# Performance work log

Measured on AMD Instinct MI355X. Metric: run time of the kernel, lower is better.

## Reference

```python
import jax, jax.numpy as jnp
import numpy as np

HIDDEN = 2048
NUM_HEADS = 16
HEAD_DIM = HIDDEN // NUM_HEADS


def setup_inputs() -> dict:
    key = jax.random.key(0)
    k1, k2, k3 = jax.random.split(key, 3)
    B, S = 2, 2048
    hidden_states = jax.random.normal(k1, (B, S, HIDDEN), dtype=jnp.float32)
    attention_mask = jnp.zeros((B, 1, 1, S), dtype=jnp.float32)
    W_qkv = jax.random.normal(k2, (HIDDEN, 3 * HIDDEN), dtype=jnp.float32) * (1.0 / np.sqrt(HIDDEN))
    b_qkv = jnp.zeros((3 * HIDDEN,), dtype=jnp.float32)
    W_out = jax.random.normal(k3, (HIDDEN, HIDDEN), dtype=jnp.float32) * (1.0 / np.sqrt(HIDDEN))
    b_out = jnp.zeros((HIDDEN,), dtype=jnp.float32)
    return {"hidden_states": hidden_states, "attention_mask": attention_mask,
            "W_qkv": W_qkv, "b_qkv": b_qkv, "W_out": W_out, "b_out": b_out}


def reference(hidden_states, attention_mask, W_qkv, b_qkv, W_out, b_out):
    B, S, H = hidden_states.shape
    scale = 1.0 / np.sqrt(HEAD_DIM)
    # fused QKV projection (column-parallel linear, world_size=1)
    mixed = hidden_states @ W_qkv + b_qkv                      # [B,S,3H]
    q, k, v = jnp.split(mixed, 3, axis=-1)
    # [B, heads, S, head_dim]
    q = q.reshape(B, S, NUM_HEADS, HEAD_DIM).transpose(0, 2, 1, 3)
    k = k.reshape(B, S, NUM_HEADS, HEAD_DIM).transpose(0, 2, 1, 3)
    v = v.reshape(B, S, NUM_HEADS, HEAD_DIM).transpose(0, 2, 1, 3)
    scores = jnp.einsum('bhqd,bhkd->bhqk', q, k) * scale       # [B,h,S,S]
    scores = scores + attention_mask                            # additive mask broadcast
    probs = jax.nn.softmax(scores, axis=-1)
    ctx = jnp.einsum('bhqk,bhkd->bhqd', probs, v)               # [B,h,S,d]
    ctx = ctx.transpose(0, 2, 1, 3).reshape(B, S, H)
    return ctx @ W_out + b_out
```

## Files before the change

### kernel.cpp

```cpp
#include <hip/hip_runtime.h>
#include <hip/hip_bf16.h>
#include <stdint.h>

typedef __attribute__((ext_vector_type(4)))  float   f32x4;
typedef __attribute__((ext_vector_type(16))) float   f32x16;
typedef __attribute__((ext_vector_type(8)))  __bf16  bf16x8;
typedef __attribute__((ext_vector_type(8)))  short   s16x8;
typedef __attribute__((ext_vector_type(4)))  unsigned short u16x4;
typedef __attribute__((ext_vector_type(4)))  float   fl4;
typedef __attribute__((ext_vector_type(2)))  unsigned int u32x2;
typedef __attribute__((ext_vector_type(4)))  unsigned int u32x4;

#define DEVFN static __device__ __forceinline__

constexpr int BATCH = 2, SEQ = 2048, HID = 2048, NHEAD = 16, HDIM = 128;
constexpr int MROWS = BATCH * SEQ;
constexpr int N3    = 3 * HID;
constexpr float LOG2E = 1.44269504088896340736f;
constexpr float SCALE_LOG2E = 0.12751649736170852f;
constexpr float DEFER_THR = 11.541560327111708f;

DEVFN unsigned short f2bf(float f) {
  unsigned int u = __float_as_uint(f);
  u += 0x7FFFu + ((u >> 16) & 1u);
  return (unsigned short)(u >> 16);
}

DEVFN void async_cp16(const void* g, void* l) {
  __builtin_amdgcn_global_load_lds(
      (__attribute__((address_space(1))) void*)g,
      (__attribute__((address_space(3))) void*)l, 16, 0, 0);
}

DEVFN f32x4 mfma_bf16(bf16x8 a, bf16x8 b, f32x4 c) {
  return __builtin_amdgcn_mfma_f32_16x16x32_bf16(a, b, c, 0, 0, 0);
}
DEVFN f32x16 mfma32(bf16x8 a, bf16x8 b, f32x16 c) {
  return __builtin_amdgcn_mfma_f32_32x32x16_bf16(a, b, c, 0, 0, 0);
}
DEVFN unsigned cvt_pk_bf16(float lo, float hi) {
  unsigned r;
  asm("v_cvt_pk_bf16_f32 %0, %1, %2" : "=v"(r) : "v"(lo), "v"(hi));
  return r;
}

__global__ __launch_bounds__(256) void cvt_bf16(const float* __restrict__ x,
                                                unsigned short* __restrict__ hi, int n4) {
  for (int i = blockIdx.x * blockDim.x + threadIdx.x; i < n4; i += gridDim.x * blockDim.x) {
    fl4 v = ((const fl4*)x)[i];
    u16x4 h;
#pragma unroll
    for (int j = 0; j < 4; j++) h[j] = f2bf(v[j]);
    ((u16x4*)hi)[i] = h;
  }
}

__global__ __launch_bounds__(256) void cvt_transpose(const float* __restrict__ W,
                                                     unsigned short* __restrict__ T,
                                                     int R, int C) {
  __shared__ float tile[32][33];
  const int c0 = blockIdx.x * 32, r0 = blockIdx.y * 32;
  const int tx = threadIdx.x, ty = threadIdx.y;
#pragma unroll
  for (int i = 0; i < 4; i++) tile[ty + 8 * i][tx] = W[(size_t)(r0 + ty + 8 * i) * C + c0 + tx];
  __syncthreads();
#pragma unroll
  for (int i = 0; i < 4; i++) {
    const float v = tile[tx][ty + 8 * i];
    T[(size_t)(c0 + ty + 8 * i) * R + r0 + tx] = f2bf(v);
  }
}

template <bool OUT_BF16>
__global__ __launch_bounds__(512, 1) void gemm_ring(const unsigned short* __restrict__ A,
                                                    const unsigned short* __restrict__ Bt,
                                                    const float* __restrict__ bias,
                                                    void* __restrict__ Cout, int Ndim) {
  constexpr int KDIM  = 2048;
  constexpr int NT    = KDIM / 64;
  constexpr int ASLOT = 256 * 64;
  constexpr int BSLOT = 128 * 64;
  constexpr int SLOT  = ASLOT + BSLOT;
  __shared__ __align__(16) unsigned short smem[3 * SLOT];

  const int tid = threadIdx.x;
  const int wid = tid >> 6, lane = tid & 63;
  const int wm = wid >> 2, wn = wid & 3;
  const int g = lane >> 4, q = lane & 15;
  const int n0 = blockIdx.x * 128, m0 = blockIdx.y * 256;

  const int srow = (wid << 3) + (lane >> 3);
  const int scol = (((lane & 7) ^ (lane >> 3)) << 4);
  const char* gA = (const char*)A  + ((size_t)(m0 + srow) * KDIM) * 2 + scol;
  const char* gB = (const char*)Bt + ((size_t)(n0 + srow) * KDIM) * 2 + scol;
  const int dbase = ((wid << 3)) << 7;

  f32x4 acc[8][2] = {};
  const int axor = (q & 7) << 4;

  auto STAGE = [&](int tt, int slot) {
    char* sA = (char*)(smem + slot * SLOT);
    char* sB = (char*)(smem + slot * SLOT + ASLOT);
    const size_t koff = (size_t)tt << 7;
#pragma unroll
    for (int i = 0; i < 4; i++)
      async_cp16(gA + (size_t)(i * 64) * (KDIM * 2) + koff, sA + dbase + (i << 13));
#pragma unroll
    for (int i = 0; i < 2; i++)
      async_cp16(gB + (size_t)(i * 64) * (KDIM * 2) + koff, sB + dbase + (i << 13));
  };

  auto COMPUTE = [&](int slot) {
    const char* sA = (const char*)(smem + slot * SLOT);
    const char* sB = (const char*)(smem + slot * SLOT + ASLOT);
#pragma unroll
    for (int ks = 0; ks < 2; ks++) {
      const int kb = (ks << 6) + (g << 4);
      bf16x8 av[8], bv[2];
#pragma unroll
      for (int nf = 0; nf < 2; nf++) {
        const int row = (wn << 5) + (nf << 4) + q;
        bv[nf] = *(const bf16x8*)(sB + (row << 7) + (kb ^ axor));
      }
#pragma unroll
      for (int mf = 0; mf < 8; mf++) {
        const int row = (wm << 7) + (mf << 4) + q;
        av[mf] = *(const bf16x8*)(sA + (row << 7) + (kb ^ axor));
      }
#pragma unroll
      for (int mf = 0; mf < 8; mf++)
#pragma unroll
        for (int nf = 0; nf < 2; nf++)
          acc[mf][nf] = mfma_bf16(av[mf], bv[nf], acc[mf][nf]);
    }
  };

  STAGE(0, 0);
  STAGE(1, 1);
  int s2 = 2, sc = 0;
#pragma unroll 1
  for (int t = 0; t < NT - 2; ++t) {
    asm volatile("s_waitcnt vmcnt(6)" ::: "memory");
    __builtin_amdgcn_s_barrier();
    asm volatile("" ::: "memory");
    STAGE(t + 2, s2);
    COMPUTE(sc);
    s2 = (s2 == 2) ? 0 : s2 + 1;
    sc = (sc == 2) ? 0 : sc + 1;
  }
  asm volatile("s_waitcnt vmcnt(6)" ::: "memory");
  __builtin_amdgcn_s_barrier();
  asm volatile("" ::: "memory");
  COMPUTE(sc);
  sc = (sc == 2) ? 0 : sc + 1;
  asm volatile("s_waitcnt vmcnt(0)" ::: "memory");
  __builtin_amdgcn_s_barrier();
  asm volatile("" ::: "memory");
  COMPUTE(sc);

  float bvv[2];
#pragma unroll
  for (int nf = 0; nf < 2; nf++) bvv[nf] = bias[n0 + (wn << 5) + (nf << 4) + q];
#pragma unroll
  for (int mf = 0; mf < 8; mf++) {
    const int rowg = m0 + (wm << 7) + (mf << 4) + (g << 2);
#pragma unroll
    for (int nf = 0; nf < 2; nf++) {
      const int colg = n0 + (wn << 5) + (nf << 4) + q;
#pragma unroll
      for (int r = 0; r < 4; r++) {
        const float v = acc[mf][nf][r] + bvv[nf];
        if (OUT_BF16)
          ((unsigned short*)Cout)[(size_t)(rowg + r) * Ndim + colg] = f2bf(v);
        else
          ((float*)Cout)[(size_t)(rowg + r) * Ndim + colg] = v;
      }
    }
  }
}

__global__ __launch_bounds__(256) void transpose_v(const unsigned short* __restrict__ qkv,
                                                   unsigned short* __restrict__ vt) {
  __shared__ __align__(16) unsigned short tile[64][136];
  const int z = blockIdx.y, b = z >> 4, h = z & 15;
  const int s0 = blockIdx.x << 6;
  const int t = threadIdx.x;
#pragma unroll
  for (int i = 0; i < 4; i++) {
    const int idx = t + (i << 8);
    const int row = idx >> 4, ch = idx & 15;
    *(s16x8*)&tile[row][ch << 3] =
        *(const s16x8*)(qkv + (size_t)(b * SEQ + s0 + row) * N3 + 2 * HID + h * HDIM + (ch << 3));
  }
  __syncthreads();
#pragma unroll
  for (int i = 0; i < 4; i++) {
    const int idx = t + (i << 8);
    const int d = idx >> 3, sc = idx & 7;
    s16x8 v;
#pragma unroll
    for (int j = 0; j < 8; j++) v[j] = (short)tile[(sc << 3) + j][d];
    *(s16x8*)(vt + (size_t)(z * HDIM + d) * SEQ + s0 + (sc << 3)) = v;
  }
}

__global__ __launch_bounds__(256, 2) void attn_kernel(const unsigned short* __restrict__ qkv,
                                                      const unsigned short* __restrict__ vt,
                                                      const float* __restrict__ mask,
                                                      unsigned short* __restrict__ ctx) {
  constexpr int NT    = SEQ / 64;
  constexpr int KSLOT = 64 * 128;
  constexpr int VSLOT = 64 * 128;
  constexpr int SLOT  = KSLOT + VSLOT;
  __shared__ __align__(16) unsigned short sKV[2 * SLOT];
  __shared__ __align__(16) float sM[SEQ];

  const int bid = blockIdx.x;
  const int idx = bid >> 3;
  const int z  = ((bid & 7) << 2) + (idx >> 4);
  const int qb = idx & 15;
  const int b = z >> 4, h = z & 15;
  const int tid = threadIdx.x, wid = tid >> 6, lane = tid & 63;
  const int l31 = lane & 31, hi = lane >> 5;
  const int q0w = (qb << 7) + (wid << 5);

#pragma unroll
  for (int j = 0; j < 2; j++) {
    fl4 m = ((const fl4*)(mask + (size_t)b * SEQ))[tid + (j << 8)];
    m *= LOG2E;
    ((fl4*)sM)[tid + (j << 8)] = m;
  }

  bf16x8 bq[8];
  {
    const char* qrow = (const char*)(qkv + (size_t)(b * SEQ + q0w + l31) * N3 + h * HDIM);
#pragma unroll
    for (int kc = 0; kc < 8; kc++) bq[kc] = *(const bf16x8*)(qrow + (kc << 5) + (hi << 4));
  }

  f32x16 acc2[4] = {};
  float mrun = -1e30f, lrun = 0.f;

  const char* gK = (const char*)qkv + ((size_t)(b * SEQ) * N3 + HID + h * HDIM) * 2;
  const char* gV = (const char*)vt + ((size_t)z * HDIM * SEQ) * 2;

  auto STAGE = [&](int tt, int slot) {
    char* kb_ = (char*)(sKV + slot * SLOT);
    char* vb_ = kb_ + KSLOT * 2;
    const int k0 = tt << 6;
#pragma unroll
    for (int i = 0; i < 4; i++) {
      const int row = (i << 4) + (wid << 2) + (lane >> 4);
      const int sl  = lane & 15;
      const int dst = (i << 12) + (wid << 10);
      async_cp16(gK + ((size_t)(k0 + row) * N3) * 2 + (((sl ^ (row & 15))) << 4),
                 kb_ + dst);
      const int sv  = sl ^ (row & 15);
      const int dhi = sv >> 3, kc8 = sv & 7;
      async_cp16(gV + ((size_t)((dhi << 6) + row) * SEQ + k0 + (kc8 << 3)) * 2,
                 vb_ + dst);
    }
  };

  auto COMPUTE = [&](int t, int slot) {
    const char* sK = (const char*)(sKV + slot * SLOT);
    const char* sV = (const char*)(sKV + slot * SLOT + KSLOT);
    const int k0 = t << 6;

    f32x16 accs[2] = {};
    __builtin_amdgcn_s_setprio(1);
#pragma unroll
    for (int kb = 0; kb < 2; kb++)
#pragma unroll
      for (int kc = 0; kc < 8; kc++) {
        const int key = (kb << 5) + l31;
        const bf16x8 ka = *(const bf16x8*)(sK + (key << 8) +
                                           ((((kc << 1) + hi) ^ (l31 & 15)) << 4));
        accs[kb] = mfma32(ka, bq[kc], accs[kb]);
      }
    __builtin_amdgcn_s_setprio(0);

    float p_[2][16];
#pragma unroll
    for (int kb = 0; kb < 2; kb++) {
      fl4 mk[4];
#pragma unroll
      for (int m = 0; m < 4; m++) mk[m] = *(const fl4*)&sM[k0 + (kb << 5) + (m << 3) + (hi << 2)];
#pragma unroll
      for (int r = 0; r < 16; r++)
        p_[kb][r] = fmaf(accs[kb][r], SCALE_LOG2E, mk[r >> 2][r & 3]);
    }
    float mt = p_[0][0];
#pragma unroll
    for (int kb = 0; kb < 2; kb++)
#pragma unroll
      for (int r = 0; r < 16; r++) mt = fmaxf(mt, p_[kb][r]);
    mt = fmaxf(mt, __shfl_xor(mt, 32));
    if (!__all(mt <= mrun + DEFER_THR)) {
      const float mnew = fmaxf(mrun, mt);
      const float fs = exp2f(mrun - mnew);
      lrun *= fs;
#pragma unroll
      for (int r = 0; r < 16; r++) {
        const int qr = (r & 3) + ((r >> 2) << 3) + (hi << 2);
        const float fr = __shfl(fs, (lane & 32) | qr);
#pragma unroll
        for (int db = 0; db < 4; db++) acc2[db][r] *= fr;
      }
      mrun = mnew;
    }
    float ps = 0.f;
#pragma unroll
    for (int kb = 0; kb < 2; kb++)
#pragma unroll
      for (int r = 0; r < 16; r++) {
        const float e = exp2f(p_[kb][r] - mrun);
        p_[kb][r] = e;
        ps += e;
      }
    ps += __shfl_xor(ps, 32);
    lrun += ps;

    bf16x8 pa[4];
#pragma unroll
    for (int kb = 0; kb < 2; kb++)
#pragma unroll
      for (int hh = 0; hh < 2; hh++) {
        const float* pp = &p_[kb][hh << 3];
        const unsigned x01 = cvt_pk_bf16(pp[0], pp[1]);
        const unsigned x23 = cvt_pk_bf16(pp[2], pp[3]);
        const unsigned y01 = cvt_pk_bf16(pp[4], pp[5]);
        const unsigned y23 = cvt_pk_bf16(pp[6], pp[7]);
        const u32x2 sa = __builtin_amdgcn_permlane32_swap(x01, y01, false, false);
        const u32x2 sb = __builtin_amdgcn_permlane32_swap(x23, y23, false, false);
        const u32x4 w = {sa[0], sb[0], sa[1], sb[1]};
        pa[(kb << 1) + hh] = __builtin_bit_cast(bf16x8, w);
      }

    __builtin_amdgcn_s_setprio(1);
#pragma unroll
    for (int db = 0; db < 4; db++) {
      const int dd = ((db & 1) << 5) + l31;
#pragma unroll
      for (int ks = 0; ks < 4; ks++) {
        const int sv = ((db >> 1) << 3) + (ks << 1) + hi;
        const bf16x8 bv = *(const bf16x8*)(sV + (dd << 8) + ((sv ^ (l31 & 15)) << 4));
        acc2[db] = mfma32(pa[ks], bv, acc2[db]);
      }
    }
    __builtin_amdgcn_s_setprio(0);
  };

  STAGE(0, 0);
  __syncthreads();
#pragma unroll 1
  for (int t = 0; t < NT - 1; ++t) {
    STAGE(t + 1, (t + 1) & 1);
    COMPUTE(t, t & 1);
    asm volatile("s_waitcnt vmcnt(0)" ::: "memory");
    __builtin_amdgcn_s_barrier();
    asm volatile("" ::: "memory");
  }
  COMPUTE(NT - 1, (NT - 1) & 1);

  const float inv = 1.f / lrun;
#pragma unroll
  for (int r = 0; r < 16; r++) {
    const int qr = (r & 3) + ((r >> 2) << 3) + (hi << 2);
    const float fr = __shfl(inv, (lane & 32) | qr);
    unsigned short* crow = ctx + (size_t)(b * SEQ + q0w + qr) * HID + h * HDIM + l31;
#pragma unroll
    for (int db = 0; db < 4; db++) crow[db << 5] = f2bf(acc2[db][r] * fr);
  }
}

extern "C" void kernel_launch(void* const* d_in, const int* in_sizes, int n_in,
                              void* d_out, int out_size, void* d_ws, size_t ws_size,
                              hipStream_t stream) {
  const float* hs   = (const float*)d_in[0];
  const float* mask = (const float*)d_in[1];
  const float* Wqkv = (const float*)d_in[2];
  const float* bqkv = (const float*)d_in[3];
  const float* Wout = (const float*)d_in[4];
  const float* bout = (const float*)d_in[5];

  char* ws = (char*)d_ws;
  size_t off = 0;
  auto alloc = [&](size_t n) { char* p = ws + off; off += (n + 255) & ~(size_t)255; return p; };
  unsigned short* hs_bf = (unsigned short*)alloc((size_t)MROWS * HID * 2);
  unsigned short* wq_bf = (unsigned short*)alloc((size_t)N3 * HID * 2);
  unsigned short* wo_bf = (unsigned short*)alloc((size_t)HID * HID * 2);
  unsigned short* qkvb  = (unsigned short*)alloc((size_t)MROWS * N3 * 2);
  unsigned short* vtb   = (unsigned short*)alloc((size_t)BATCH * NHEAD * HDIM * SEQ * 2);
  unsigned short* ctxb  = (unsigned short*)alloc((size_t)MROWS * HID * 2);
  (void)ws_size;

  cvt_bf16<<<2048, 256, 0, stream>>>(hs, hs_bf, MROWS * HID / 4);
  dim3 tb(32, 8);
  cvt_transpose<<<dim3(N3 / 32, HID / 32), tb, 0, stream>>>(Wqkv, wq_bf, HID, N3);
  cvt_transpose<<<dim3(HID / 32, HID / 32), tb, 0, stream>>>(Wout, wo_bf, HID, HID);
  gemm_ring<true ><<<dim3(N3 / 128, MROWS / 256), 512, 0, stream>>>(hs_bf, wq_bf, bqkv, qkvb, N3);
  transpose_v<<<dim3(SEQ / 64, BATCH * NHEAD), 256, 0, stream>>>(qkvb, vtb);
  attn_kernel<<<512, 256, 0, stream>>>(qkvb, vtb, mask, ctxb);
  gemm_ring<false><<<dim3(HID / 128, MROWS / 256), 512, 0, stream>>>(ctxb, wo_bf, bout, (float*)d_out, HID);
}
```

Before: 267.1 us.

## Interleave GEMM tile staging with MFMA phases using ping-pong barriers and priorities

Splits the GEMM compute into four phases, each loading its A fragments from LDS, issuing part of the next tile's async global-to-LDS copies, then running MFMAs at raised wave priority between barriers. The aim is to spread memory issue across the compute so loads overlap MFMA work instead of being issued in one burst before it. The cost is several extra barriers and full lgkmcnt waits per k-step, which may serialize waves and reduce latency hiding.

New measurement: 270.4 us. Within noise of the previous version (+1.2%).

```diff
diff --git a/kernel.cpp b/kernel.cpp
--- a/kernel.cpp
+++ b/kernel.cpp
@@ -110,28 +110,53 @@
       async_cp16(gB + (size_t)(i * 64) * (KDIM * 2) + koff, sB + dbase + (i << 13));
   };
 
-  auto COMPUTE = [&](int slot) {
+  auto COMPUTE = [&](int slot, int tstage, int sstage, bool doStage) {
     const char* sA = (const char*)(smem + slot * SLOT);
     const char* sB = (const char*)(smem + slot * SLOT + ASLOT);
-#pragma unroll
-    for (int ks = 0; ks < 2; ks++) {
-      const int kb = (ks << 6) + (g << 4);
-      bf16x8 av[8], bv[2];
-#pragma unroll
-      for (int nf = 0; nf < 2; nf++) {
-        const int row = (wn << 5) + (nf << 4) + q;
-        bv[nf] = *(const bf16x8*)(sB + (row << 7) + (kb ^ axor));
-      }
-#pragma unroll
-      for (int mf = 0; mf < 8; mf++) {
-        const int row = (wm << 7) + (mf << 4) + q;
-        av[mf] = *(const bf16x8*)(sA + (row << 7) + (kb ^ axor));
-      }
-#pragma unroll
-      for (int mf = 0; mf < 8; mf++)
+    char* snA = (char*)(smem + sstage * SLOT);
+    char* snB = (char*)(smem + sstage * SLOT + ASLOT);
+    const size_t koff = (size_t)tstage << 7;
+    bf16x8 bv[2][2];
+#pragma unroll
+    for (int p = 0; p < 4; p++) {
+      if (p == 0) {
 #pragma unroll
         for (int nf = 0; nf < 2; nf++)
-          acc[mf][nf] = mfma_bf16(av[mf], bv[nf], acc[mf][nf]);
+#pragma unroll
+          for (int kk = 0; kk < 2; kk++) {
+            const int row = (wn << 5) + (nf << 4) + q;
+            bv[nf][kk] = *(const bf16x8*)(sB + (row << 7) + (((kk << 6) + (g << 4)) ^ axor));
+          }
+      }
+      bf16x8 av[2][2];
+#pragma unroll
+      for (int i = 0; i < 2; i++)
+#pragma unroll
+        for (int kk = 0; kk < 2; kk++) {
+          const int row = (wm << 7) + (((p << 1) + i) << 4) + q;
+          av[i][kk] = *(const bf16x8*)(sA + (row << 7) + (((kk << 6) + (g << 4)) ^ axor));
+        }
+      if (doStage) {
+        if (p < 2) {
+          async_cp16(gA + (size_t)((p * 2) * 64) * (KDIM * 2) + koff, snA + dbase + ((p * 2) << 13));
+          async_cp16(gA + (size_t)((p * 2 + 1) * 64) * (KDIM * 2) + koff, snA + dbase + ((p * 2 + 1) << 13));
+        } else {
+          async_cp16(gB + (size_t)((p - 2) * 64) * (KDIM * 2) + koff, snB + dbase + ((p - 2) << 13));
+        }
+      }
+      __builtin_amdgcn_s_barrier();
+      asm volatile("s_waitcnt lgkmcnt(0)" ::: "memory");
+      __builtin_amdgcn_sched_barrier(0);
+      __builtin_amdgcn_s_setprio(1);
+#pragma unroll
+      for (int i = 0; i < 2; i++)
+#pragma unroll
+        for (int nf = 0; nf < 2; nf++)
+#pragma unroll
+          for (int kk = 0; kk < 2; kk++)
+            acc[(p << 1) + i][nf] = mfma_bf16(av[i][kk], bv[nf][kk], acc[(p << 1) + i][nf]);
+      __builtin_amdgcn_s_setprio(0);
+      __builtin_amdgcn_s_barrier();
     }
   };
 
@@ -143,20 +168,19 @@
     asm volatile("s_waitcnt vmcnt(6)" ::: "memory");
     __builtin_amdgcn_s_barrier();
     asm volatile("" ::: "memory");
-    STAGE(t + 2, s2);
-    COMPUTE(sc);
+    COMPUTE(sc, t + 2, s2, true);
     s2 = (s2 == 2) ? 0 : s2 + 1;
     sc = (sc == 2) ? 0 : sc + 1;
   }
   asm volatile("s_waitcnt vmcnt(6)" ::: "memory");
   __builtin_amdgcn_s_barrier();
   asm volatile("" ::: "memory");
-  COMPUTE(sc);
+  COMPUTE(sc, 0, s2, false);
   sc = (sc == 2) ? 0 : sc + 1;
   asm volatile("s_waitcnt vmcnt(0)" ::: "memory");
   __builtin_amdgcn_s_barrier();
   asm volatile("" ::: "memory");
-  COMPUTE(sc);
+  COMPUTE(sc, 0, s2, false);
 
   float bvv[2];
 #pragma unroll
@@ -253,12 +277,10 @@
       const int row = (i << 4) + (wid << 2) + (lane >> 4);
       const int sl  = lane & 15;
       const int dst = (i << 12) + (wid << 10);
-      async_cp16(gK + ((size_t)(k0 + row) * N3) * 2 + (((sl ^ (row & 15))) << 4),
-                 kb_ + dst);
+      async_cp16(gK + ((size_t)(k0 + row) * N3) * 2 + (((sl ^ (row & 15))) << 4), kb_ + dst);
       const int sv  = sl ^ (row & 15);
       const int dhi = sv >> 3, kc8 = sv & 7;
-      async_cp16(gV + ((size_t)((dhi << 6) + row) * SEQ + k0 + (kc8 << 3)) * 2,
-                 vb_ + dst);
+      async_cp16(gV + ((size_t)((dhi << 6) + row) * SEQ + k0 + (kc8 << 3)) * 2, vb_ + dst);
     }
   };
 
```
